# Optimization experiments

Measured on AMD Instinct MI355X. Metric: run time of the kernel, lower is better.

Reference implementation:

```python
import jax, jax.numpy as jnp
import numpy as np

D = 1024
LN_EPS = 1e-5


def setup_inputs() -> dict:
    key = jax.random.key(0)
    k1, k2 = jax.random.split(key)
    L, B = 2048, 8
    x = jax.random.normal(k1, (L, B, D), dtype=jnp.float32)
    c = jnp.zeros((B, D), dtype=jnp.float32)
    W = jax.random.normal(k2, (3 * D, D), dtype=jnp.float32) * (1.0 / np.sqrt(D))
    # bias: forget-gate slice [D:2D] initialized to 1.5, rest zero (matches _init_bias)
    b = jnp.zeros((3 * D,), dtype=jnp.float32).at[D:2 * D].set(1.5)
    ln_g = jnp.ones((D,), dtype=jnp.float32)
    ln_b = jnp.zeros((D,), dtype=jnp.float32)
    return {"x": x, "c": c, "W": W, "b": b, "ln_g": ln_g, "ln_b": ln_b}


def _layernorm(x, g, b):
    mu = jnp.mean(x, axis=-1, keepdims=True)
    var = jnp.mean(jnp.square(x - mu), axis=-1, keepdims=True)
    return (x - mu) * jax.lax.rsqrt(var + LN_EPS) * g + b


def _sru_forward(x, c, W, b, ln_g, ln_b):
    residual = x
    x_norm = _layernorm(x, ln_g, ln_b)          # [L, B, D]
    ufr = jnp.einsum('lbd,ed->lbe', x_norm, W) + b  # [L, B, 3D]
    u, f, r = jnp.split(ufr, 3, axis=-1)
    f_gate = jax.nn.sigmoid(f)
    r_gate = jax.nn.sigmoid(r)
    u_tanh = jnp.tanh(u)

    def step(c_prev, inputs):
        f_t, u_t = inputs
        c_t = f_t * c_prev + (1.0 - f_t) * u_t
        return c_t, c_t

    last_c, c_stack = jax.lax.scan(step, c, (f_gate, u_tanh))  # [L, B, D]
    hs = r_gate * jnp.tanh(c_stack) + (1.0 - r_gate) * x_norm
    return residual + hs, last_c


def reference(x, c, W, b, ln_g, ln_b):
    return _sru_forward(x, c, W, b, ln_g, ln_b)
```

## Files before the change

### kernel.cpp

```cpp
#include <hip/hip_runtime.h>

#define L_DIM 2048
#define B_DIM 8
#define DD    1024
#define M_DIM 16384
#define N_DIM 3072
#define K_DIM 1024
#define CH    8192
#define CH8   1024
#define NSEG  128
#define LSEG  16
#define LN_EPS 1e-5f

typedef __attribute__((ext_vector_type(8))) short bf16x8;
typedef __attribute__((ext_vector_type(8))) unsigned short u16x8;
typedef __attribute__((ext_vector_type(4))) float f32x4;

__device__ __forceinline__ unsigned short f2bf(float f){
  unsigned u = __float_as_uint(f);
  u += 0x7fffu + ((u >> 16) & 1u);
  return (unsigned short)(u >> 16);
}
__device__ __forceinline__ float bf2f(unsigned short h){
  return __uint_as_float(((unsigned)h) << 16);
}
__device__ __forceinline__ float fsigmoid(float z){ return 1.0f/(1.0f + __expf(-z)); }
__device__ __forceinline__ float ftanh(float z){ return 1.0f - 2.0f/(1.0f + __expf(2.0f*z)); }

__global__ __launch_bounds__(256) void ln_kernel(const float* __restrict__ x,
                                                 const float* __restrict__ g,
                                                 const float* __restrict__ bta,
                                                 unsigned short* __restrict__ xn)
{
  int tid  = threadIdx.x;
  int wave = tid >> 6, lane = tid & 63;
  int row  = blockIdx.x * 4 + wave;
  const float4* xr = (const float4*)(x + (size_t)row * DD);
  float4 v[4];
  #pragma unroll
  for (int k = 0; k < 4; k++) v[k] = xr[lane + k * 64];
  float s = 0.f, sq = 0.f;
  #pragma unroll
  for (int k = 0; k < 4; k++) {
    s  += v[k].x + v[k].y + v[k].z + v[k].w;
    sq += v[k].x*v[k].x + v[k].y*v[k].y + v[k].z*v[k].z + v[k].w*v[k].w;
  }
  #pragma unroll
  for (int off = 32; off > 0; off >>= 1) {
    s  += __shfl_down(s,  off, 64);
    sq += __shfl_down(sq, off, 64);
  }
  s  = __shfl(s,  0, 64);
  sq = __shfl(sq, 0, 64);
  float mean = s * (1.0f / DD);
  float var  = sq * (1.0f / DD) - mean * mean;
  float rstd = rsqrtf(var + LN_EPS);
  ushort4* xo = (ushort4*)(xn + (size_t)row * DD);
  #pragma unroll
  for (int k = 0; k < 4; k++) {
    float4 gg = ((const float4*)g)[lane + k * 64];
    float4 bb = ((const float4*)bta)[lane + k * 64];
    ushort4 o;
    o.x = f2bf((v[k].x - mean) * rstd * gg.x + bb.x);
    o.y = f2bf((v[k].y - mean) * rstd * gg.y + bb.y);
    o.z = f2bf((v[k].z - mean) * rstd * gg.z + bb.z);
    o.w = f2bf((v[k].w - mean) * rstd * gg.w + bb.w);
    xo[lane + k * 64] = o;
  }
}

__global__ __launch_bounds__(256) void wconv_kernel(const float* __restrict__ W,
                                                    unsigned short* __restrict__ wb)
{
  int gid = blockIdx.x * 256 + threadIdx.x;
  float4 v = ((const float4*)W)[gid];
  ushort4 o;
  o.x = f2bf(v.x); o.y = f2bf(v.y); o.z = f2bf(v.z); o.w = f2bf(v.w);
  ((ushort4*)wb)[gid] = o;
}

#define BM 128
#define BN 128
#define BK 64
#define LDP 136

#define GLDS16(gp, lp) __builtin_amdgcn_global_load_lds( \
    (const __attribute__((address_space(1))) void*)(gp), \
    (__attribute__((address_space(3))) void*)(lp), 16, 0, 0)

__global__ __launch_bounds__(256) void gemm_gates(const unsigned short* __restrict__ A,
                                                  const unsigned short* __restrict__ Bw,
                                                  const float* __restrict__ bias,
                                                  unsigned short* __restrict__ u_t,
                                                  unsigned short* __restrict__ f_g,
                                                  unsigned short* __restrict__ r_g)
{
  __shared__ unsigned short smem[BM * LDP];
  unsigned short* sA = smem;
  unsigned short* sB = smem + BM * BK;
  int tid  = threadIdx.x;
  int wave = tid >> 6, lane = tid & 63;
  int bm0 = blockIdx.x * BM;
  int bn0 = blockIdx.y * BN;

  f32x4 zero = {0.f, 0.f, 0.f, 0.f};
  f32x4 acc[4][4];
  #pragma unroll
  for (int i = 0; i < 4; i++)
    #pragma unroll
    for (int j = 0; j < 4; j++) acc[i][j] = zero;

  int q8  = lane >> 3;
  int rr8 = lane & 7;
  int sch = rr8 ^ q8;
  const unsigned short* a_lane = A  + (size_t)(bm0 + wave * 32 + q8) * K_DIM + sch * 8;
  const unsigned short* b_lane = Bw + (size_t)(bn0 + wave * 32 + q8) * K_DIM + sch * 8;

  int wm = (wave & 1) * 64, wn = (wave >> 1) * 64;
  int fm = lane & 15, quad = lane >> 4;
  int f7 = fm & 7;

  for (int k0 = 0; k0 < K_DIM; k0 += BK) {
    #pragma unroll
    for (int i = 0; i < 4; i++) {
      GLDS16(a_lane + (size_t)(i * 8) * K_DIM + k0, &sA[(wave * 32 + i * 8) * BK]);
      GLDS16(b_lane + (size_t)(i * 8) * K_DIM + k0, &sB[(wave * 32 + i * 8) * BK]);
    }
    __syncthreads();

    #pragma unroll
    for (int kk = 0; kk < 2; kk++) {
      bf16x8 af[4], bfr[4];
      #pragma unroll
      for (int i = 0; i < 4; i++) {
        int slot = (kk * 4 + quad) ^ f7;
        af[i]  = *(const bf16x8*)&sA[(wm + i * 16 + fm) * BK + slot * 8];
        bfr[i] = *(const bf16x8*)&sB[(wn + i * 16 + fm) * BK + slot * 8];
      }
      #pragma unroll
      for (int mi = 0; mi < 4; mi++)
        #pragma unroll
        for (int ni = 0; ni < 4; ni++)
          acc[mi][ni] = __builtin_amdgcn_mfma_f32_16x16x32_bf16(af[mi], bfr[ni], acc[mi][ni], 0, 0, 0);
    }
    __syncthreads();
  }

  int slice = bn0 >> 10;
  int nd0   = bn0 & 1023;
  unsigned short* dst = (slice == 0) ? u_t : ((slice == 1) ? f_g : r_g);

  #pragma unroll
  for (int ni = 0; ni < 4; ni++) {
    int lcol = wn + ni * 16 + fm;
    float bia = bias[bn0 + lcol];
    #pragma unroll
    for (int mi = 0; mi < 4; mi++) {
      #pragma unroll
      for (int reg = 0; reg < 4; reg++) {
        int lrow = wm + mi * 16 + quad * 4 + reg;
        float v = acc[mi][ni][reg] + bia;
        float act = (slice == 0) ? ftanh(v) : fsigmoid(v);
        smem[lrow * LDP + lcol] = f2bf(act);
      }
    }
  }
  __syncthreads();

  #pragma unroll
  for (int it = 0; it < 8; it++) {
    int row = it * 16 + (tid >> 4);
    int cc  = (tid & 15) * 8;
    u16x8 v = *(const u16x8*)&smem[row * LDP + cc];
    *(u16x8*)(dst + (size_t)(bm0 + row) * DD + nd0 + cc) = v;
  }
}

__global__ __launch_bounds__(256) void scan_pass1(const unsigned short* __restrict__ f_g,
                                                  const unsigned short* __restrict__ u_t,
                                                  unsigned short* __restrict__ P,
                                                  unsigned short* __restrict__ E)
{
  int vc8 = blockIdx.x * 256 + threadIdx.x;
  int seg = blockIdx.y;
  const u16x8* f8 = (const u16x8*)f_g;
  const u16x8* u8 = (const u16x8*)u_t;
  size_t g = (size_t)(seg * LSEG) * CH8 + vc8;
  float p[8], e[8];
  #pragma unroll
  for (int k = 0; k < 8; k++) { p[k] = 1.f; e[k] = 0.f; }
  #pragma unroll 4
  for (int i = 0; i < LSEG; i++) {
    u16x8 ff = f8[g];
    u16x8 uu = u8[g];
    #pragma unroll
    for (int k = 0; k < 8; k++) {
      float fv = bf2f(ff[k]);
      e[k] = fv * e[k] + (1.f - fv) * bf2f(uu[k]);
      p[k] *= fv;
    }
    g += CH8;
  }
  u16x8 pv, ev;
  #pragma unroll
  for (int k = 0; k < 8; k++) { pv[k] = f2bf(p[k]); ev[k] = f2bf(e[k]); }
  ((u16x8*)P)[(size_t)seg * CH8 + vc8] = pv;
  ((u16x8*)E)[(size_t)seg * CH8 + vc8] = ev;
}

__global__ __launch_bounds__(128) void scan_pass2(const unsigned short* __restrict__ P,
                                                  const unsigned short* __restrict__ E,
                                                  const float* __restrict__ c0,
                                                  float* __restrict__ Cini,
                                                  float* __restrict__ lastc)
{
  int ch = blockIdx.x * 128 + threadIdx.x;
  float c = c0[ch];
  #pragma unroll 8
  for (int s = 0; s < NSEG; s++) {
    Cini[(size_t)s * CH + ch] = c;
    c = bf2f(P[(size_t)s * CH + ch]) * c + bf2f(E[(size_t)s * CH + ch]);
  }
  lastc[ch] = c;
}

__global__ __launch_bounds__(256) void scan_pass3(const unsigned short* __restrict__ f_g,
                                                  const unsigned short* __restrict__ u_t,
                                                  const unsigned short* __restrict__ r_g,
                                                  const float* __restrict__ x,
                                                  const unsigned short* __restrict__ xn,
                                                  const float* __restrict__ Cini,
                                                  float* __restrict__ out)
{
  int vc8 = blockIdx.x * 256 + threadIdx.x;
  int seg = blockIdx.y;
  const u16x8* f8 = (const u16x8*)f_g;
  const u16x8* u8 = (const u16x8*)u_t;
  const u16x8* r8 = (const u16x8*)r_g;
  const u16x8* n8 = (const u16x8*)xn;
  const float4* x4 = (const float4*)x;
  float4* o4 = (float4*)out;
  float c[8];
  {
    const float4* C4 = (const float4*)Cini;
    size_t ci = (size_t)seg * (CH / 4) + (size_t)vc8 * 2;
    float4 ca = C4[ci], cb = C4[ci + 1];
    c[0]=ca.x; c[1]=ca.y; c[2]=ca.z; c[3]=ca.w;
    c[4]=cb.x; c[5]=cb.y; c[6]=cb.z; c[7]=cb.w;
  }
  size_t g = (size_t)(seg * LSEG) * CH8 + vc8;
  #pragma unroll 2
  for (int i = 0; i < LSEG; i++) {
    u16x8 ff = f8[g];
    u16x8 uu = u8[g];
    u16x8 rr = r8[g];
    u16x8 nn = n8[g];
    size_t xi = g * 2;
    float4 xa = x4[xi], xb = x4[xi + 1];
    float ov[8];
    #pragma unroll
    for (int k = 0; k < 8; k++) {
      float fv = bf2f(ff[k]);
      c[k] = fv * c[k] + (1.f - fv) * bf2f(uu[k]);
      float rv = bf2f(rr[k]);
      ov[k] = rv * ftanh(c[k]) + (1.f - rv) * bf2f(nn[k]);
    }
    o4[xi]     = (float4){xa.x + ov[0], xa.y + ov[1], xa.z + ov[2], xa.w + ov[3]};
    o4[xi + 1] = (float4){xb.x + ov[4], xb.y + ov[5], xb.z + ov[6], xb.w + ov[7]};
    g += CH8;
  }
}

extern "C" void kernel_launch(void* const* d_in, const int* in_sizes, int n_in,
                              void* d_out, int out_size, void* d_ws, size_t ws_size,
                              hipStream_t stream) {
  const float* x    = (const float*)d_in[0];
  const float* c0   = (const float*)d_in[1];
  const float* W    = (const float*)d_in[2];
  const float* bias = (const float*)d_in[3];
  const float* ln_g = (const float*)d_in[4];
  const float* ln_b = (const float*)d_in[5];
  float* out = (float*)d_out;

  char* ws = (char*)d_ws;
  unsigned short* xn  = (unsigned short*)(ws);
  unsigned short* wb  = (unsigned short*)(ws + 33554432ULL);
  unsigned short* u_t = (unsigned short*)(ws + 39845888ULL);
  unsigned short* f_g = (unsigned short*)(ws + 73400320ULL);
  unsigned short* r_g = (unsigned short*)(ws + 106954752ULL);
  unsigned short* Pseg = (unsigned short*)(ws + 33554432ULL);
  unsigned short* Eseg = (unsigned short*)(ws + 35651584ULL);
  float* Cini = (float*)(ws + 140509184ULL);

  ln_kernel   <<<M_DIM / 4, 256, 0, stream>>>(x, ln_g, ln_b, xn);
  wconv_kernel<<<N_DIM, 256, 0, stream>>>(W, wb);
  gemm_gates  <<<dim3(M_DIM / BM, N_DIM / BN), 256, 0, stream>>>(xn, wb, bias, u_t, f_g, r_g);
  scan_pass1  <<<dim3(CH8 / 256, NSEG), 256, 0, stream>>>(f_g, u_t, Pseg, Eseg);
  scan_pass2  <<<CH / 128, 128, 0, stream>>>(Pseg, Eseg, c0, Cini, out + (size_t)M_DIM * DD);
  scan_pass3  <<<dim3(CH8 / 256, NSEG), 256, 0, stream>>>(f_g, u_t, r_g, x, xn, Cini, out);
}
```

Measured before the change: 224.3 us.

## Rewrite gates GEMM as 256x256 double-buffered pipelined tile with 8 waves

Replaces the 128x128 single-buffered GEMM with a 256x256 tile using 512 threads, double-buffered LDS staging via global_load_lds and explicit interleaving of loads, barriers and MFMA quarters with priority hints. This is meant to hide global load latency behind MFMA work and to raise operand reuse per LDS byte. The epilogue is split into two halves to fit the padded output tile in LDS. It uses 128KB of LDS and many accumulator registers, which may limit occupancy. The grid drops to 64x12 blocks, which may reduce load balance across CUs.

After: 235.6 us. +5.0%, slower.

```diff
diff --git a/kernel.cpp b/kernel.cpp
--- a/kernel.cpp
+++ b/kernel.cpp
@@ -79,100 +79,159 @@
   ((ushort4*)wb)[gid] = o;
 }
 
-#define BM 128
-#define BN 128
+#define BM 256
+#define BN 256
 #define BK 64
-#define LDP 136
+#define NT 16
+#define LDPE 264
 
 #define GLDS16(gp, lp) __builtin_amdgcn_global_load_lds( \
     (const __attribute__((address_space(1))) void*)(gp), \
     (__attribute__((address_space(3))) void*)(lp), 16, 0, 0)
 
-__global__ __launch_bounds__(256) void gemm_gates(const unsigned short* __restrict__ A,
-                                                  const unsigned short* __restrict__ Bw,
-                                                  const float* __restrict__ bias,
-                                                  unsigned short* __restrict__ u_t,
-                                                  unsigned short* __restrict__ f_g,
-                                                  unsigned short* __restrict__ r_g)
-{
-  __shared__ unsigned short smem[BM * LDP];
-  unsigned short* sA = smem;
-  unsigned short* sB = smem + BM * BK;
-  int tid  = threadIdx.x;
-  int wave = tid >> 6, lane = tid & 63;
-  int bm0 = blockIdx.x * BM;
-  int bn0 = blockIdx.y * BN;
+#define SBAR()   __builtin_amdgcn_s_barrier()
+#define SCHED0() __builtin_amdgcn_sched_barrier(0)
+#define WAIT_LGKM0() do { asm volatile("s_waitcnt lgkmcnt(0)" ::: "memory"); SCHED0(); } while(0)
+#define WAIT_VM(N)   do { asm volatile("s_waitcnt vmcnt(" #N ")" ::: "memory"); SCHED0(); } while(0)
+
+__global__ __launch_bounds__(512, 2) void gemm_gates(const unsigned short* __restrict__ Ag,
+                                                     const unsigned short* __restrict__ Bg,
+                                                     const float* __restrict__ bias,
+                                                     unsigned short* __restrict__ u_t,
+                                                     unsigned short* __restrict__ f_g,
+                                                     unsigned short* __restrict__ r_g)
+{
+  __shared__ unsigned short smem[65536];
+  const int tid  = threadIdx.x;
+  const int wave = tid >> 6, lane = tid & 63;
+  const int wm = wave >> 2, wn = wave & 3;
+  const int r8 = lane >> 3;
+  const int sch = (lane & 7) ^ r8;
+  const int fm = lane & 15, quad = lane >> 4, f7 = fm & 7;
+  const int bm0 = blockIdx.x * BM, bn0 = blockIdx.y * BN;
 
   f32x4 zero = {0.f, 0.f, 0.f, 0.f};
-  f32x4 acc[4][4];
-  #pragma unroll
-  for (int i = 0; i < 4; i++)
+  f32x4 acc[8][4];
+  #pragma unroll
+  for (int i = 0; i < 8; i++)
     #pragma unroll
     for (int j = 0; j < 4; j++) acc[i][j] = zero;
 
-  int q8  = lane >> 3;
-  int rr8 = lane & 7;
-  int sch = rr8 ^ q8;
-  const unsigned short* a_lane = A  + (size_t)(bm0 + wave * 32 + q8) * K_DIM + sch * 8;
-  const unsigned short* b_lane = Bw + (size_t)(bn0 + wave * 32 + q8) * K_DIM + sch * 8;
-
-  int wm = (wave & 1) * 64, wn = (wave >> 1) * 64;
-  int fm = lane & 15, quad = lane >> 4;
-  int f7 = fm & 7;
-
-  for (int k0 = 0; k0 < K_DIM; k0 += BK) {
-    #pragma unroll
-    for (int i = 0; i < 4; i++) {
-      GLDS16(a_lane + (size_t)(i * 8) * K_DIM + k0, &sA[(wave * 32 + i * 8) * BK]);
-      GLDS16(b_lane + (size_t)(i * 8) * K_DIM + k0, &sB[(wave * 32 + i * 8) * BK]);
+#define STAGE_A(BUF, T, HALF) do { \
+  GLDS16(Ag + (size_t)(bm0 + (HALF)*128 + wave*16 + 0 + r8) * K_DIM + ((T)*BK + sch*8), \
+         &smem[(BUF)*16384 + ((HALF)*128 + wave*16 + 0) * 64]); \
+  GLDS16(Ag + (size_t)(bm0 + (HALF)*128 + wave*16 + 8 + r8) * K_DIM + ((T)*BK + sch*8), \
+         &smem[(BUF)*16384 + ((HALF)*128 + wave*16 + 8) * 64]); \
+} while(0)
+
+#define STAGE_B(BUF, T, HALF) do { \
+  GLDS16(Bg + (size_t)(bn0 + (HALF)*128 + wave*16 + 0 + r8) * K_DIM + ((T)*BK + sch*8), \
+         &smem[32768 + (BUF)*16384 + ((HALF)*128 + wave*16 + 0) * 64]); \
+  GLDS16(Bg + (size_t)(bn0 + (HALF)*128 + wave*16 + 8 + r8) * K_DIM + ((T)*BK + sch*8), \
+         &smem[32768 + (BUF)*16384 + ((HALF)*128 + wave*16 + 8) * 64]); \
+} while(0)
+
+#define LOAD_A(MH) do { \
+  _Pragma("unroll") for (int i_ = 0; i_ < 4; ++i_) \
+  _Pragma("unroll") for (int kk_ = 0; kk_ < 2; ++kk_) \
+    a_[i_][kk_] = *(const bf16x8*)&smem[cb*16384 + \
+        (wm*128 + (MH)*64 + i_*16 + fm)*64 + (((kk_*4 + quad) ^ f7))*8]; \
+} while(0)
+
+#define LOAD_B(NH, DEST) do { \
+  _Pragma("unroll") for (int j_ = 0; j_ < 2; ++j_) \
+  _Pragma("unroll") for (int kk_ = 0; kk_ < 2; ++kk_) \
+    DEST[j_][kk_] = *(const bf16x8*)&smem[32768 + cb*16384 + \
+        (wn*64 + (NH)*32 + j_*16 + fm)*64 + (((kk_*4 + quad) ^ f7))*8]; \
+} while(0)
+
+#define QMFMA(MH, NH, BREG) do { \
+  _Pragma("unroll") for (int i_ = 0; i_ < 4; ++i_) \
+  _Pragma("unroll") for (int j_ = 0; j_ < 2; ++j_) \
+  _Pragma("unroll") for (int kk_ = 0; kk_ < 2; ++kk_) \
+    acc[(MH)*4 + i_][(NH)*2 + j_] = __builtin_amdgcn_mfma_f32_16x16x32_bf16( \
+        a_[i_][kk_], BREG[j_][kk_], acc[(MH)*4 + i_][(NH)*2 + j_], 0, 0, 0); \
+} while(0)
+
+  bf16x8 a_[4][2], b0_[2][2], b1_[2][2];
+
+  STAGE_A(0, 0, 0); STAGE_A(0, 0, 1);
+  STAGE_B(0, 0, 0); STAGE_B(0, 0, 1);
+  STAGE_B(1, 1, 0); STAGE_B(1, 1, 1);
+  WAIT_VM(4);
+  SBAR();
+
+  for (int t = 0; t < NT; ++t) {
+    const int cb = t & 1, nb = cb ^ 1;
+    LOAD_A(0);
+    LOAD_B(0, b0_);
+    if (t + 1 < NT) STAGE_A(nb, t + 1, 0);
+    SCHED0(); SBAR();
+    WAIT_LGKM0();
+    __builtin_amdgcn_s_setprio(1);
+    QMFMA(0, 0, b0_);
+    __builtin_amdgcn_s_setprio(0);
+    SBAR();
+    LOAD_B(1, b1_);
+    if (t + 1 < NT) STAGE_A(nb, t + 1, 1);
+    SCHED0(); SBAR();
+    WAIT_LGKM0();
+    __builtin_amdgcn_s_setprio(1);
+    QMFMA(0, 1, b1_);
+    __builtin_amdgcn_s_setprio(0);
+    SBAR();
+    LOAD_A(1);
+    if (t + 2 < NT) STAGE_B(cb, t + 2, 0);
+    SCHED0(); SBAR();
+    WAIT_LGKM0();
+    __builtin_amdgcn_s_setprio(1);
+    QMFMA(1, 1, b1_);
+    __builtin_amdgcn_s_setprio(0);
+    SBAR();
+    if (t + 2 < NT) STAGE_B(cb, t + 2, 1);
+    SCHED0();
+    if (t < NT - 2)       WAIT_VM(4);
+    else if (t == NT - 2) WAIT_VM(0);
+    SBAR();
+    __builtin_amdgcn_s_setprio(1);
+    QMFMA(1, 0, b0_);
+    __builtin_amdgcn_s_setprio(0);
+    SBAR();
+  }
+  __syncthreads();
+
+  const int slice = bn0 >> 10;
+  const int nd0   = bn0 & 1023;
+  unsigned short* dst = (slice == 0) ? u_t : ((slice == 1) ? f_g : r_g);
+
+  #pragma unroll
+  for (int h = 0; h < 2; ++h) {
+    if (wm == h) {
+      #pragma unroll
+      for (int ni = 0; ni < 4; ++ni) {
+        int lcol = wn * 64 + ni * 16 + fm;
+        float bia = bias[bn0 + lcol];
+        #pragma unroll
+        for (int mi = 0; mi < 8; ++mi) {
+          #pragma unroll
+          for (int reg = 0; reg < 4; ++reg) {
+            int lrow = mi * 16 + quad * 4 + reg;
+            float v = acc[mi][ni][reg] + bia;
+            float act = (slice == 0) ? ftanh(v) : fsigmoid(v);
+            smem[lrow * LDPE + lcol] = f2bf(act);
+          }
+        }
+      }
     }
     __syncthreads();
-
     #pragma unroll
-    for (int kk = 0; kk < 2; kk++) {
-      bf16x8 af[4], bfr[4];
-      #pragma unroll
-      for (int i = 0; i < 4; i++) {
-        int slot = (kk * 4 + quad) ^ f7;
-        af[i]  = *(const bf16x8*)&sA[(wm + i * 16 + fm) * BK + slot * 8];
-        bfr[i] = *(const bf16x8*)&sB[(wn + i * 16 + fm) * BK + slot * 8];
-      }
-      #pragma unroll
-      for (int mi = 0; mi < 4; mi++)
-        #pragma unroll
-        for (int ni = 0; ni < 4; ni++)
-          acc[mi][ni] = __builtin_amdgcn_mfma_f32_16x16x32_bf16(af[mi], bfr[ni], acc[mi][ni], 0, 0, 0);
+    for (int it = 0; it < 8; ++it) {
+      int row = it * 16 + (tid >> 5);
+      int cc  = (tid & 31) * 8;
+      u16x8 v = *(const u16x8*)&smem[row * LDPE + cc];
+      *(u16x8*)(dst + (size_t)(bm0 + h * 128 + row) * DD + nd0 + cc) = v;
     }
     __syncthreads();
-  }
-
-  int slice = bn0 >> 10;
-  int nd0   = bn0 & 1023;
-  unsigned short* dst = (slice == 0) ? u_t : ((slice == 1) ? f_g : r_g);
-
-  #pragma unroll
-  for (int ni = 0; ni < 4; ni++) {
-    int lcol = wn + ni * 16 + fm;
-    float bia = bias[bn0 + lcol];
-    #pragma unroll
-    for (int mi = 0; mi < 4; mi++) {
-      #pragma unroll
-      for (int reg = 0; reg < 4; reg++) {
-        int lrow = wm + mi * 16 + quad * 4 + reg;
-        float v = acc[mi][ni][reg] + bia;
-        float act = (slice == 0) ? ftanh(v) : fsigmoid(v);
-        smem[lrow * LDP + lcol] = f2bf(act);
-      }
-    }
-  }
-  __syncthreads();
-
-  #pragma unroll
-  for (int it = 0; it < 8; it++) {
-    int row = it * 16 + (tid >> 4);
-    int cc  = (tid & 15) * 8;
-    u16x8 v = *(const u16x8*)&smem[row * LDP + cc];
-    *(u16x8*)(dst + (size_t)(bm0 + row) * DD + nd0 + cc) = v;
   }
 }
 
@@ -294,7 +353,7 @@
 
   ln_kernel   <<<M_DIM / 4, 256, 0, stream>>>(x, ln_g, ln_b, xn);
   wconv_kernel<<<N_DIM, 256, 0, stream>>>(W, wb);
-  gemm_gates  <<<dim3(M_DIM / BM, N_DIM / BN), 256, 0, stream>>>(xn, wb, bias, u_t, f_g, r_g);
+  gemm_gates  <<<dim3(M_DIM / BM, N_DIM / BN), 512, 0, stream>>>(xn, wb, bias, u_t, f_g, r_g);
   scan_pass1  <<<dim3(CH8 / 256, NSEG), 256, 0, stream>>>(f_g, u_t, Pseg, Eseg);
   scan_pass2  <<<CH / 128, 128, 0, stream>>>(Pseg, Eseg, c0, Cini, out + (size_t)M_DIM * DD);
   scan_pass3  <<<dim3(CH8 / 256, NSEG), 256, 0, stream>>>(f_g, u_t, r_g, x, xn, Cini, out);
```

## Restructure gate GEMM with triple-buffered LDS pipeline and 256x128 tiles

Applied to the files above, without the earlier changes.

Rewrites the gate GEMM to use 512-thread blocks on 256x128 tiles with BK=32 and a three-stage LDS ring buffer. Global-to-LDS loads for tile t+2 are issued while tile t is computed, using explicit vmcnt waits, raw ds_read_b128, sched barriers and setprio around the MFMA block. The aim is to overlap memory latency with MFMA work and cut per-k-step barrier stalls. The epilogue is serialized over four row groups through a smaller LDS staging area, which adds extra barriers. The LDS swizzle is dropped, which risks bank conflicts on the fragment reads.

Measured after the change: 243.5 us. +8.5%, slower.

```diff
diff --git a/kernel.cpp b/kernel.cpp
--- a/kernel.cpp
+++ b/kernel.cpp
@@ -79,29 +79,38 @@
   ((ushort4*)wb)[gid] = o;
 }
 
-#define BM 128
+#define BM 256
 #define BN 128
-#define BK 64
+#define BK 32
+#define NT 32
+#define BUFS 12288
 #define LDP 136
 
 #define GLDS16(gp, lp) __builtin_amdgcn_global_load_lds( \
     (const __attribute__((address_space(1))) void*)(gp), \
     (__attribute__((address_space(3))) void*)(lp), 16, 0, 0)
 
-__global__ __launch_bounds__(256) void gemm_gates(const unsigned short* __restrict__ A,
-                                                  const unsigned short* __restrict__ Bw,
-                                                  const float* __restrict__ bias,
-                                                  unsigned short* __restrict__ u_t,
-                                                  unsigned short* __restrict__ f_g,
-                                                  unsigned short* __restrict__ r_g)
-{
-  __shared__ unsigned short smem[BM * LDP];
-  unsigned short* sA = smem;
-  unsigned short* sB = smem + BM * BK;
-  int tid  = threadIdx.x;
-  int wave = tid >> 6, lane = tid & 63;
-  int bm0 = blockIdx.x * BM;
-  int bn0 = blockIdx.y * BN;
+#define SBAR()   __builtin_amdgcn_s_barrier()
+#define SCHED0() __builtin_amdgcn_sched_barrier(0)
+#define WAIT_LGKM0() do { asm volatile("s_waitcnt lgkmcnt(0)" ::: "memory"); SCHED0(); } while(0)
+#define WAIT_VM(N)   do { asm volatile("s_waitcnt vmcnt(" #N ")" ::: "memory"); SCHED0(); } while(0)
+
+#define DSR(dst, addr, IMM) \
+  asm volatile("ds_read_b128 %0, %1 offset:" #IMM : "=v"(dst) : "v"(addr))
+
+__global__ __launch_bounds__(512, 4) void gemm_gates(const unsigned short* __restrict__ A,
+                                                     const unsigned short* __restrict__ Bw,
+                                                     const float* __restrict__ bias,
+                                                     unsigned short* __restrict__ u_t,
+                                                     unsigned short* __restrict__ f_g,
+                                                     unsigned short* __restrict__ r_g)
+{
+  __shared__ unsigned short smem[3 * BUFS];
+  const int tid  = threadIdx.x;
+  const int wave = tid >> 6, lane = tid & 63;
+  const int wmI = wave >> 1, wnI = wave & 1;
+  const int fm = lane & 15, quad = lane >> 4;
+  const int bm0 = blockIdx.x * BM, bn0 = blockIdx.y * BN;
 
   f32x4 zero = {0.f, 0.f, 0.f, 0.f};
   f32x4 acc[4][4];
@@ -110,69 +119,84 @@
     #pragma unroll
     for (int j = 0; j < 4; j++) acc[i][j] = zero;
 
-  int q8  = lane >> 3;
-  int rr8 = lane & 7;
-  int sch = rr8 ^ q8;
-  const unsigned short* a_lane = A  + (size_t)(bm0 + wave * 32 + q8) * K_DIM + sch * 8;
-  const unsigned short* b_lane = Bw + (size_t)(bn0 + wave * 32 + q8) * K_DIM + sch * 8;
-
-  int wm = (wave & 1) * 64, wn = (wave >> 1) * 64;
-  int fm = lane & 15, quad = lane >> 4;
-  int f7 = fm & 7;
-
-  for (int k0 = 0; k0 < K_DIM; k0 += BK) {
-    #pragma unroll
-    for (int i = 0; i < 4; i++) {
-      GLDS16(a_lane + (size_t)(i * 8) * K_DIM + k0, &sA[(wave * 32 + i * 8) * BK]);
-      GLDS16(b_lane + (size_t)(i * 8) * K_DIM + k0, &sB[(wave * 32 + i * 8) * BK]);
-    }
-    __syncthreads();
-
-    #pragma unroll
-    for (int kk = 0; kk < 2; kk++) {
-      bf16x8 af[4], bfr[4];
+  const int srow = lane >> 2, schk = lane & 3;
+  const unsigned short* aS = A  + (size_t)(bm0 + wave * 32 + srow) * K_DIM + schk * 8;
+  const unsigned short* bS = Bw + (size_t)(bn0 + wave * 16 + srow) * K_DIM + schk * 8;
+
+#define STAGE(SOFF, T) do { \
+  GLDS16(aS + (T) * BK,                      &smem[(SOFF) + (wave * 32 +  0) * BK]); \
+  GLDS16(aS + (T) * BK + (size_t)16 * K_DIM, &smem[(SOFF) + (wave * 32 + 16) * BK]); \
+  GLDS16(bS + (T) * BK,                      &smem[(SOFF) + 8192 + (wave * 16) * BK]); \
+} while(0)
+
+  const unsigned aFrag = (unsigned)((wmI * 64 + fm) * 64 + quad * 16);
+  const unsigned bFrag = (unsigned)(16384 + (wnI * 64 + fm) * 64 + quad * 16);
+
+  bf16x8 a_[4], b_[4];
+
+  STAGE(0, 0);
+  STAGE(BUFS, 1);
+  WAIT_VM(3);
+  SBAR();
+
+  unsigned s0 = 0, s1 = BUFS, s2 = 2 * BUFS;
+  #pragma unroll
+  for (int t = 0; t < NT; ++t) {
+    if (t + 2 < NT) STAGE(s2, t + 2);
+    SCHED0();
+    {
+      unsigned aA = s0 * 2 + aFrag, bA = s0 * 2 + bFrag;
+      DSR(a_[0], aA, 0); DSR(a_[1], aA, 1024); DSR(a_[2], aA, 2048); DSR(a_[3], aA, 3072);
+      DSR(b_[0], bA, 0); DSR(b_[1], bA, 1024); DSR(b_[2], bA, 2048); DSR(b_[3], bA, 3072);
+    }
+    SCHED0();
+    WAIT_LGKM0();
+    __builtin_amdgcn_s_setprio(1);
+    #pragma unroll
+    for (int mi = 0; mi < 4; mi++)
       #pragma unroll
-      for (int i = 0; i < 4; i++) {
-        int slot = (kk * 4 + quad) ^ f7;
-        af[i]  = *(const bf16x8*)&sA[(wm + i * 16 + fm) * BK + slot * 8];
-        bfr[i] = *(const bf16x8*)&sB[(wn + i * 16 + fm) * BK + slot * 8];
-      }
-      #pragma unroll
-      for (int mi = 0; mi < 4; mi++)
-        #pragma unroll
-        for (int ni = 0; ni < 4; ni++)
-          acc[mi][ni] = __builtin_amdgcn_mfma_f32_16x16x32_bf16(af[mi], bfr[ni], acc[mi][ni], 0, 0, 0);
-    }
-    __syncthreads();
-  }
+      for (int ni = 0; ni < 4; ni++)
+        acc[mi][ni] = __builtin_amdgcn_mfma_f32_16x16x32_bf16(a_[mi], b_[ni], acc[mi][ni], 0, 0, 0);
+    __builtin_amdgcn_s_setprio(0);
+    SCHED0();
+    if (t < NT - 2) { WAIT_VM(3); } else { WAIT_VM(0); }
+    SBAR();
+    unsigned tmp = s0; s0 = s1; s1 = s2; s2 = tmp;
+  }
+  __syncthreads();
 
   int slice = bn0 >> 10;
   int nd0   = bn0 & 1023;
   unsigned short* dst = (slice == 0) ? u_t : ((slice == 1) ? f_g : r_g);
 
   #pragma unroll
-  for (int ni = 0; ni < 4; ni++) {
-    int lcol = wn + ni * 16 + fm;
-    float bia = bias[bn0 + lcol];
-    #pragma unroll
-    for (int mi = 0; mi < 4; mi++) {
+  for (int h = 0; h < 4; ++h) {
+    if (wmI == h) {
       #pragma unroll
-      for (int reg = 0; reg < 4; reg++) {
-        int lrow = wm + mi * 16 + quad * 4 + reg;
-        float v = acc[mi][ni][reg] + bia;
-        float act = (slice == 0) ? ftanh(v) : fsigmoid(v);
-        smem[lrow * LDP + lcol] = f2bf(act);
+      for (int ni = 0; ni < 4; ni++) {
+        int lcol = wnI * 64 + ni * 16 + fm;
+        float bia = bias[bn0 + lcol];
+        #pragma unroll
+        for (int mi = 0; mi < 4; mi++) {
+          #pragma unroll
+          for (int reg = 0; reg < 4; reg++) {
+            int lrow = mi * 16 + quad * 4 + reg;
+            float v = acc[mi][ni][reg] + bia;
+            float act = (slice == 0) ? ftanh(v) : fsigmoid(v);
+            smem[lrow * LDP + lcol] = f2bf(act);
+          }
+        }
       }
     }
-  }
-  __syncthreads();
-
-  #pragma unroll
-  for (int it = 0; it < 8; it++) {
-    int row = it * 16 + (tid >> 4);
-    int cc  = (tid & 15) * 8;
-    u16x8 v = *(const u16x8*)&smem[row * LDP + cc];
-    *(u16x8*)(dst + (size_t)(bm0 + row) * DD + nd0 + cc) = v;
+    __syncthreads();
+    #pragma unroll
+    for (int it = 0; it < 2; ++it) {
+      int row = it * 32 + (tid >> 4);
+      int cc  = (tid & 15) * 8;
+      u16x8 v = *(const u16x8*)&smem[row * LDP + cc];
+      *(u16x8*)(dst + (size_t)(bm0 + h * 64 + row) * DD + nd0 + cc) = v;
+    }
+    __syncthreads();
   }
 }
 
@@ -294,7 +318,7 @@
 
   ln_kernel   <<<M_DIM / 4, 256, 0, stream>>>(x, ln_g, ln_b, xn);
   wconv_kernel<<<N_DIM, 256, 0, stream>>>(W, wb);
-  gemm_gates  <<<dim3(M_DIM / BM, N_DIM / BN), 256, 0, stream>>>(xn, wb, bias, u_t, f_g, r_g);
+  gemm_gates  <<<dim3(M_DIM / BM, N_DIM / BN), 512, 0, stream>>>(xn, wb, bias, u_t, f_g, r_g);
   scan_pass1  <<<dim3(CH8 / 256, NSEG), 256, 0, stream>>>(f_g, u_t, Pseg, Eseg);
   scan_pass2  <<<CH / 128, 128, 0, stream>>>(Pseg, Eseg, c0, Cini, out + (size_t)M_DIM * DD);
   scan_pass3  <<<dim3(CH8 / 256, NSEG), 256, 0, stream>>>(f_g, u_t, r_g, x, xn, Cini, out);
```
